# Performance work log

Measured on AMD Instinct MI355X. Metric: run time of the kernel, lower is better.

The kernel has to match this reference:

```python
import jax, jax.numpy as jnp
import numpy as np


def _sage_layer(x, neighbors, W, b):
    # x: (N, D), neighbors: (N, deg) int indices into x
    neigh_agg = x[neighbors].mean(axis=1)           # (N, D) gather + mean
    h = jnp.concatenate([x, neigh_agg], axis=-1)     # (N, 2D)
    return jax.nn.relu(h @ W + b)                    # (N, D_out)


def setup_inputs() -> dict:
    key = jax.random.key(0)
    k1, k2, k3, k4 = jax.random.split(key, 4)
    N, D, DEG = 50000, 128, 16
    x = jax.random.normal(k1, (N, D), dtype=jnp.float32)
    neighbors = jax.random.randint(k2, (N, DEG), 0, N)
    # Linear(in_dim*2, out_dim) weights, stored as (2D, D_out) for x @ W
    scale = 1.0 / np.sqrt(2 * D)
    W1 = jax.random.normal(k3, (2 * D, D), dtype=jnp.float32) * scale
    b1 = jnp.zeros((D,), dtype=jnp.float32)
    W2 = jax.random.normal(k4, (2 * D, D), dtype=jnp.float32) * scale
    b2 = jnp.zeros((D,), dtype=jnp.float32)
    return {"x": x, "neighbors": neighbors, "W1": W1, "b1": b1, "W2": W2, "b2": b2}


def reference(x, neighbors, W1, b1, W2, b2):
    h = _sage_layer(x, neighbors, W1, b1)
    h = _sage_layer(h, neighbors, W2, b2)
    return h
```

## Files before the change

kernel.cpp:

```cpp
#include <hip/hip_runtime.h>
#include <hip/hip_bf16.h>

typedef __attribute__((ext_vector_type(8))) short short8;
typedef __attribute__((ext_vector_type(4))) float f32x4;

#define N_NODES 50000
#define D 128
#define DEG 16
#define K2 256
#define BM 32

static __device__ __forceinline__ unsigned short f2b(float f) {
    union { float f; unsigned int u; } v; v.f = f;
    return (unsigned short)((v.u + 0x7fffu + ((v.u >> 16) & 1u)) >> 16);
}
static __device__ __forceinline__ float b2f(unsigned short u) {
    union { unsigned int u; float f; } v; v.u = ((unsigned int)u) << 16;
    return v.f;
}

__global__ void prep(const float* __restrict__ x, unsigned short* __restrict__ xb,
                     const float* __restrict__ W1, const float* __restrict__ W2,
                     unsigned short* __restrict__ Wt1, unsigned short* __restrict__ Wt2) {
    int b = blockIdx.x;
    if (b < 128) {
        int i = b * 256 + threadIdx.x;
        int k = i / D, n = i % D;
        Wt1[n * K2 + k] = f2b(W1[i]);
        Wt2[n * K2 + k] = f2b(W2[i]);
    } else {
        int i = ((b - 128) * 256 + threadIdx.x) * 4;
        if (i < N_NODES * D) {
            float4 v = *(const float4*)(x + i);
            ushort4 o;
            o.x = f2b(v.x); o.y = f2b(v.y); o.z = f2b(v.z); o.w = f2b(v.w);
            *(ushort4*)(xb + i) = o;
        }
    }
}

template <int OUT_BF16>
__global__ __launch_bounds__(256, 4)
void sage_layer(const unsigned short* __restrict__ feat,
                const int* __restrict__ nbr,
                const unsigned short* __restrict__ wt,
                const float* __restrict__ bias,
                void* __restrict__ out)
{
    __shared__ __align__(16) unsigned short Hl[BM * 264];
    __shared__ int Nl[BM * DEG];
    const int tid  = threadIdx.x;
    const int row0 = blockIdx.x * BM;

    if (tid < 128) {
        int g = row0 * DEG + tid * 4;
        int gmax = N_NODES * DEG - 4;
        if (g > gmax) g = gmax;
        *(int4*)(Nl + tid * 4) = *(const int4*)(nbr + g);
    }
    __syncthreads();

    #pragma unroll
    for (int p = 0; p < 2; ++p) {
        int a = tid + p * 256;
        int r = a >> 4;
        int s = a & 15;
        int grow = row0 + r;
        if (grow >= N_NODES) grow = N_NODES - 1;
        const unsigned short* sp = feat + (size_t)grow * D + s * 8;
        short8 self = *(const short8*)sp;

        int4 i0 = *(const int4*)(Nl + r * 16);
        int4 i1 = *(const int4*)(Nl + r * 16 + 4);
        int4 i2 = *(const int4*)(Nl + r * 16 + 8);
        int4 i3 = *(const int4*)(Nl + r * 16 + 12);
        int ids[16] = { i0.x, i0.y, i0.z, i0.w, i1.x, i1.y, i1.z, i1.w,
                        i2.x, i2.y, i2.z, i2.w, i3.x, i3.y, i3.z, i3.w };

        short8 v[16];
        #pragma unroll
        for (int j = 0; j < 16; ++j)
            v[j] = *(const short8*)(feat + (size_t)ids[j] * D + s * 8);

        float am[8];
        #pragma unroll
        for (int i = 0; i < 8; ++i) am[i] = 0.f;
        #pragma unroll
        for (int j = 0; j < 16; ++j)
            #pragma unroll
            for (int i = 0; i < 8; ++i)
                am[i] += b2f((unsigned short)v[j][i]);

        unsigned short* hr = Hl + r * 264 + s * 8;
        *(short8*)(hr) = self;
        short8 m;
        #pragma unroll
        for (int i = 0; i < 8; ++i) m[i] = (short)f2b(am[i] * 0.0625f);
        *(short8*)(hr + D) = m;
    }

    const int lane = tid & 63;
    const int w    = tid >> 6;
    const int quad = lane >> 4;
    const int l16  = lane & 15;
    const int n_base = w * 32;
    short8 bfrag[8][2];
    #pragma unroll
    for (int kk = 0; kk < 8; ++kk)
        #pragma unroll
        for (int ct = 0; ct < 2; ++ct)
            bfrag[kk][ct] = *(const short8*)(wt + (n_base + ct * 16 + l16) * K2 + kk * 32 + quad * 8);

    __syncthreads();

    f32x4 acc[2][2];
    #pragma unroll
    for (int rt = 0; rt < 2; ++rt)
        #pragma unroll
        for (int ct = 0; ct < 2; ++ct)
            acc[rt][ct] = (f32x4){0.f, 0.f, 0.f, 0.f};

    #pragma unroll
    for (int kk = 0; kk < 8; ++kk) {
        short8 afrag[2];
        #pragma unroll
        for (int rt = 0; rt < 2; ++rt)
            afrag[rt] = *(const short8*)(&Hl[(rt * 16 + l16) * 264 + kk * 32 + quad * 8]);
        #pragma unroll
        for (int rt = 0; rt < 2; ++rt)
            #pragma unroll
            for (int ct = 0; ct < 2; ++ct)
                acc[rt][ct] = __builtin_amdgcn_mfma_f32_16x16x32_bf16(
                    afrag[rt], bfrag[kk][ct], acc[rt][ct], 0, 0, 0);
    }

    float bv0 = bias[n_base + l16];
    float bv1 = bias[n_base + 16 + l16];
    #pragma unroll
    for (int rt = 0; rt < 2; ++rt) {
        int grow_base = row0 + rt * 16 + quad * 4;
        #pragma unroll
        for (int r = 0; r < 4; ++r) {
            int grow = grow_base + r;
            if (grow >= N_NODES) continue;
            #pragma unroll
            for (int ct = 0; ct < 2; ++ct) {
                float vv = acc[rt][ct][r] + (ct ? bv1 : bv0);
                vv = vv > 0.f ? vv : 0.f;
                int col = n_base + ct * 16 + l16;
                if (OUT_BF16)
                    ((unsigned short*)out)[grow * D + col] = f2b(vv);
                else
                    ((float*)out)[grow * D + col] = vv;
            }
        }
    }
}

extern "C" void kernel_launch(void* const* d_in, const int* in_sizes, int n_in,
                              void* d_out, int out_size, void* d_ws, size_t ws_size,
                              hipStream_t stream) {
    const float* x  = (const float*)d_in[0];
    const int*   nb = (const int*)d_in[1];
    const float* W1 = (const float*)d_in[2];
    const float* b1 = (const float*)d_in[3];
    const float* W2 = (const float*)d_in[4];
    const float* b2 = (const float*)d_in[5];

    char* ws = (char*)d_ws;
    unsigned short* Wt1 = (unsigned short*)(ws);
    unsigned short* Wt2 = (unsigned short*)(ws + 65536);
    unsigned short* xb  = (unsigned short*)(ws + 131072);
    unsigned short* h1  = (unsigned short*)(ws + 131072 + 12800000);

    prep<<<128 + 6250, 256, 0, stream>>>(x, xb, W1, W2, Wt1, Wt2);

    const int mgrid = (N_NODES + BM - 1) / BM;
    sage_layer<1><<<mgrid, 256, 0, stream>>>(xb, nb, Wt1, b1, h1);
    sage_layer<0><<<mgrid, 256, 0, stream>>>(h1, nb, Wt2, b2, d_out);
}
```

Baseline: 156.0 us.

## Pre-swizzle weights into MFMA fragment order and pack bf16 accumulation

The prep kernel now writes the bf16 weights directly in the per-wave MFMA B-fragment order, so each lane's fragment load in the layer kernel is a contiguous coalesced 16-byte read instead of a strided gather. Gather address arithmetic switches to 32-bit byte offsets with shifts, and the neighbor mean unpacks bf16 pairs into float2 vectors, which may allow packed float adds. The weight prep uses fewer threads, but each thread does strided reads of W.

```diff
diff --git a/kernel.cpp b/kernel.cpp
--- a/kernel.cpp
+++ b/kernel.cpp
@@ -1,8 +1,8 @@
 #include <hip/hip_runtime.h>
-#include <hip/hip_bf16.h>
 
 typedef __attribute__((ext_vector_type(8))) short short8;
 typedef __attribute__((ext_vector_type(4))) float f32x4;
+typedef __attribute__((ext_vector_type(2))) float f32x2;
 
 #define N_NODES 50000
 #define D 128
@@ -14,27 +14,38 @@
     union { float f; unsigned int u; } v; v.f = f;
     return (unsigned short)((v.u + 0x7fffu + ((v.u >> 16) & 1u)) >> 16);
 }
-static __device__ __forceinline__ float b2f(unsigned short u) {
-    union { unsigned int u; float f; } v; v.u = ((unsigned int)u) << 16;
-    return v.f;
-}
 
 __global__ void prep(const float* __restrict__ x, unsigned short* __restrict__ xb,
                      const float* __restrict__ W1, const float* __restrict__ W2,
-                     unsigned short* __restrict__ Wt1, unsigned short* __restrict__ Wt2) {
+                     unsigned short* __restrict__ Wf1, unsigned short* __restrict__ Wf2) {
     int b = blockIdx.x;
-    if (b < 128) {
-        int i = b * 256 + threadIdx.x;
-        int k = i / D, n = i % D;
-        Wt1[n * K2 + k] = f2b(W1[i]);
-        Wt2[n * K2 + k] = f2b(W2[i]);
+    if (b < 32) {
+        int o  = (b * 256 + threadIdx.x) * 4;
+        int e0 = o & 7;
+        int l  = (o >> 3) & 63;
+        int ct = (o >> 9) & 1;
+        int kk = (o >> 10) & 7;
+        int w  = o >> 13;
+        int n  = w * 32 + ct * 16 + (l & 15);
+        int kb = kk * 32 + (l >> 4) * 8 + e0;
+        ushort4 a, c;
+        a.x = f2b(W1[(kb + 0) * D + n]);
+        a.y = f2b(W1[(kb + 1) * D + n]);
+        a.z = f2b(W1[(kb + 2) * D + n]);
+        a.w = f2b(W1[(kb + 3) * D + n]);
+        *(ushort4*)(Wf1 + o) = a;
+        c.x = f2b(W2[(kb + 0) * D + n]);
+        c.y = f2b(W2[(kb + 1) * D + n]);
+        c.z = f2b(W2[(kb + 2) * D + n]);
+        c.w = f2b(W2[(kb + 3) * D + n]);
+        *(ushort4*)(Wf2 + o) = c;
     } else {
-        int i = ((b - 128) * 256 + threadIdx.x) * 4;
+        int i = ((b - 32) * 256 + threadIdx.x) * 4;
         if (i < N_NODES * D) {
             float4 v = *(const float4*)(x + i);
-            ushort4 o;
-            o.x = f2b(v.x); o.y = f2b(v.y); o.z = f2b(v.z); o.w = f2b(v.w);
-            *(ushort4*)(xb + i) = o;
+            ushort4 o4;
+            o4.x = f2b(v.x); o4.y = f2b(v.y); o4.z = f2b(v.z); o4.w = f2b(v.w);
+            *(ushort4*)(xb + i) = o4;
         }
     }
 }
@@ -43,7 +54,7 @@
 __global__ __launch_bounds__(256, 4)
 void sage_layer(const unsigned short* __restrict__ feat,
                 const int* __restrict__ nbr,
-                const unsigned short* __restrict__ wt,
+                const unsigned short* __restrict__ wf,
                 const float* __restrict__ bias,
                 void* __restrict__ out)
 {
@@ -60,6 +71,8 @@
     }
     __syncthreads();
 
+    const char* fb = (const char*)feat;
+
     #pragma unroll
     for (int p = 0; p < 2; ++p) {
         int a = tid + p * 256;
@@ -67,8 +80,8 @@
         int s = a & 15;
         int grow = row0 + r;
         if (grow >= N_NODES) grow = N_NODES - 1;
-        const unsigned short* sp = feat + (size_t)grow * D + s * 8;
-        short8 self = *(const short8*)sp;
+        unsigned sB = (unsigned)s * 16u;
+        short8 self = *(const short8*)(fb + (unsigned)grow * 256u + sB);
 
         int4 i0 = *(const int4*)(Nl + r * 16);
         int4 i1 = *(const int4*)(Nl + r * 16 + 4);
@@ -80,23 +93,33 @@
         short8 v[16];
         #pragma unroll
         for (int j = 0; j < 16; ++j)
-            v[j] = *(const short8*)(feat + (size_t)ids[j] * D + s * 8);
-
-        float am[8];
-        #pragma unroll
-        for (int i = 0; i < 8; ++i) am[i] = 0.f;
-        #pragma unroll
-        for (int j = 0; j < 16; ++j)
+            v[j] = *(const short8*)(fb + (((unsigned)ids[j]) << 8) + sB);
+
+        f32x2 am[4];
+        #pragma unroll
+        for (int i = 0; i < 4; ++i) am[i] = (f32x2){0.f, 0.f};
+        #pragma unroll
+        for (int j = 0; j < 16; ++j) {
+            union { short8 s8; unsigned u[4]; } vv; vv.s8 = v[j];
             #pragma unroll
-            for (int i = 0; i < 8; ++i)
-                am[i] += b2f((unsigned short)v[j][i]);
+            for (int i = 0; i < 4; ++i) {
+                unsigned ui = vv.u[i];
+                f32x2 e;
+                e.x = __uint_as_float(ui << 16);
+                e.y = __uint_as_float(ui & 0xffff0000u);
+                am[i] += e;
+            }
+        }
 
         unsigned short* hr = Hl + r * 264 + s * 8;
         *(short8*)(hr) = self;
-        short8 m;
-        #pragma unroll
-        for (int i = 0; i < 8; ++i) m[i] = (short)f2b(am[i] * 0.0625f);
-        *(short8*)(hr + D) = m;
+        union { unsigned short u[8]; short8 s8; } m;
+        #pragma unroll
+        for (int i = 0; i < 4; ++i) {
+            m.u[2 * i]     = f2b(am[i].x * 0.0625f);
+            m.u[2 * i + 1] = f2b(am[i].y * 0.0625f);
+        }
+        *(short8*)(hr + D) = m.s8;
     }
 
     const int lane = tid & 63;
@@ -104,12 +127,13 @@
     const int quad = lane >> 4;
     const int l16  = lane & 15;
     const int n_base = w * 32;
+    const unsigned short* wfw = wf + w * 8192;
     short8 bfrag[8][2];
     #pragma unroll
     for (int kk = 0; kk < 8; ++kk)
         #pragma unroll
         for (int ct = 0; ct < 2; ++ct)
-            bfrag[kk][ct] = *(const short8*)(wt + (n_base + ct * 16 + l16) * K2 + kk * 32 + quad * 8);
+            bfrag[kk][ct] = *(const short8*)(wfw + kk * 1024 + ct * 512 + lane * 8);
 
     __syncthreads();
 
@@ -168,14 +192,14 @@
     const float* b2 = (const float*)d_in[5];
 
     char* ws = (char*)d_ws;
-    unsigned short* Wt1 = (unsigned short*)(ws);
-    unsigned short* Wt2 = (unsigned short*)(ws + 65536);
+    unsigned short* Wf1 = (unsigned short*)(ws);
+    unsigned short* Wf2 = (unsigned short*)(ws + 65536);
     unsigned short* xb  = (unsigned short*)(ws + 131072);
     unsigned short* h1  = (unsigned short*)(ws + 131072 + 12800000);
 
-    prep<<<128 + 6250, 256, 0, stream>>>(x, xb, W1, W2, Wt1, Wt2);
+    prep<<<32 + 6250, 256, 0, stream>>>(x, xb, W1, W2, Wf1, Wf2);
 
     const int mgrid = (N_NODES + BM - 1) / BM;
-    sage_layer<1><<<mgrid, 256, 0, stream>>>(xb, nb, Wt1, b1, h1);
-    sage_layer<0><<<mgrid, 256, 0, stream>>>(h1, nb, Wt2, b2, d_out);
-}
+    sage_layer<1><<<mgrid, 256, 0, stream>>>(xb, nb, Wf1, b1, h1);
+    sage_layer<0><<<mgrid, 256, 0, stream>>>(h1, nb, Wf2, b2, d_out);
+}
```

Result: faster. 144.1 us (-7.6%).
